# Optimization experiments

Measured on AMD Instinct MI355X. Metric: run time of the kernel, lower is better.

The kernel has to match this reference:

```python
import jax, jax.numpy as jnp
import numpy as np

B, N, D, E = 2, 50000, 128, 800000
EPS = 1e-5


def layer_norm(x, gamma, beta):
    m = jnp.mean(x, axis=-1, keepdims=True)
    v = jnp.mean((x - m) ** 2, axis=-1, keepdims=True)
    return (x - m) * jax.lax.rsqrt(v + EPS) * gamma + beta


def setup_inputs() -> dict:
    key = jax.random.key(0)
    ks = jax.random.split(key, 8)
    x = jax.random.normal(ks[0], (B, N, D), dtype=jnp.float32)
    edge_src = jax.random.randint(ks[1], (E,), 0, N)
    edge_dst = jax.random.randint(ks[2], (E,), 0, N)
    # degree consistent with edge_dst (in-degree), as a float tensor
    degree = jax.ops.segment_sum(jnp.ones((E,), jnp.float32), edge_dst, num_segments=N)
    # LayerNorm params (torch default init: gamma=1, beta=0)
    sn_g = jnp.ones((D,), jnp.float32); sn_b = jnp.zeros((D,), jnp.float32)
    nn_g = jnp.ones((D,), jnp.float32); nn_b = jnp.zeros((D,), jnp.float32)
    # MLP: Linear(2D, 2D) -> GELU -> Linear(2D, D); stored as [in, out]
    s1 = 1.0 / np.sqrt(2 * D)
    W1 = jax.random.uniform(ks[3], (2 * D, 2 * D), jnp.float32, -s1, s1)
    b1 = jax.random.uniform(ks[4], (2 * D,), jnp.float32, -s1, s1)
    W2 = jax.random.uniform(ks[5], (2 * D, D), jnp.float32, -s1, s1)
    b2 = jax.random.uniform(ks[6], (D,), jnp.float32, -s1, s1)
    return {"x": x, "edge_src": edge_src, "edge_dst": edge_dst, "degree": degree,
            "sn_g": sn_g, "sn_b": sn_b, "nn_g": nn_g, "nn_b": nn_b,
            "W1": W1, "b1": b1, "W2": W2, "b2": b2}


def reference(x, edge_src, edge_dst, degree, sn_g, sn_b, nn_g, nn_b, W1, b1, W2, b2):
    # gather messages from source nodes, scatter-add into destination nodes
    neighbor = jnp.zeros_like(x).at[:, edge_dst, :].add(x[:, edge_src, :])  # [B,N,D]
    neighbor = neighbor / jnp.clip(degree, 1.0)[None, :, None]
    h = jnp.concatenate([layer_norm(x, sn_g, sn_b), layer_norm(neighbor, nn_g, nn_b)], axis=-1)  # [B,N,2D]
    h = jax.nn.gelu(h @ W1 + b1, approximate=False)  # torch nn.GELU default = exact erf
    return x + (h @ W2 + b2)
```

## Files before the change

kernel.cpp:

```cpp
#include <hip/hip_runtime.h>
#include <cstdint>

#define B_ 2
#define N_ 50000
#define D_ 128
#define E_ 800000
#define TOK 100000

typedef __bf16 bf16x8 __attribute__((ext_vector_type(8)));
typedef float f32x4 __attribute__((ext_vector_type(4)));

__device__ __forceinline__ unsigned short f2bf(float f) {
  union { float f; uint32_t u; } v; v.f = f;
  uint32_t u = v.u;
  return (unsigned short)((u + 0x7FFFu + ((u >> 16) & 1u)) >> 16);
}
__device__ __forceinline__ float uasf(uint32_t u) {
  union { uint32_t u; float f; } v; v.u = u; return v.f;
}
__device__ __forceinline__ float fast_gelu(float v) {
  float p = v * (1.5957691f + 0.07135481f * v * v);
  return v * __builtin_amdgcn_rcpf(1.0f + __expf(-p));
}

__global__ __launch_bounds__(256) void prep_k(
    const float* __restrict__ x, const float* __restrict__ W1,
    const float* __restrict__ W2, const float* __restrict__ degree,
    unsigned short* __restrict__ xb, unsigned short* __restrict__ W1t,
    unsigned short* __restrict__ W2t, int* __restrict__ rs,
    int* __restrict__ cursor) {
  __shared__ int wsum[4], woff[4], carry[2];
  const int blk = blockIdx.x;
  if (blk < 12500) {
    int q = (blk * 256 + threadIdx.x) * 4;
    int node = q >> 8;
    int rem = q & 255;
    int b = rem >> 7, c = rem & 127;
    float4 v = *(const float4*)(x + (size_t)b * (N_ * D_) + node * 128 + c);
    uint2 p = { (uint32_t)f2bf(v.x) | ((uint32_t)f2bf(v.y) << 16),
                (uint32_t)f2bf(v.z) | ((uint32_t)f2bf(v.w) << 16) };
    *(uint2*)(xb + q) = p;
  } else if (blk < 12884) {
    int t = (blk - 12500) * 256 + threadIdx.x;
    if (t < 65536) {
      int n = t >> 8, k = t & 255;
      int f = (n >> 4) * 8 + (k >> 5);
      int pos = ((n & 15) + ((k >> 3) & 3) * 16) * 8 + (k & 7);
      W1t[f * 512 + pos] = f2bf(W1[k * 256 + n]);
    } else {
      int t2 = t - 65536;
      int n = t2 >> 8, k = t2 & 255;
      int f = (n >> 4) * 8 + (k >> 5);
      int pos = ((n & 15) + ((k >> 3) & 3) * 16) * 8 + (k & 7);
      W2t[f * 512 + pos] = f2bf(W2[k * 128 + n]);
    }
  } else {
    const int tid = threadIdx.x, lane = tid & 63, wv = tid >> 6;
    if (tid == 0) carry[0] = 0;
    int p = 0;
    __syncthreads();
    for (int base = 0; base < N_; base += 1024) {
      int i = base + tid * 4;
      int4 v = {0, 0, 0, 0};
      if (i + 3 < N_) {
        float4 d4 = *(const float4*)(degree + i);
        v.x = (int)(d4.x + 0.5f); v.y = (int)(d4.y + 0.5f);
        v.z = (int)(d4.z + 0.5f); v.w = (int)(d4.w + 0.5f);
      } else {
        if (i     < N_) v.x = (int)(degree[i]     + 0.5f);
        if (i + 1 < N_) v.y = (int)(degree[i + 1] + 0.5f);
        if (i + 2 < N_) v.z = (int)(degree[i + 2] + 0.5f);
        if (i + 3 < N_) v.w = (int)(degree[i + 3] + 0.5f);
      }
      int s4 = v.x + v.y + v.z + v.w;
      int s = s4;
#pragma unroll
      for (int off = 1; off < 64; off <<= 1) {
        int t = __shfl_up(s, off);
        if (lane >= off) s += t;
      }
      if (lane == 63) wsum[wv] = s;
      __syncthreads();
      if (tid == 0) {
        int a = 0;
#pragma unroll
        for (int w = 0; w < 4; ++w) { woff[w] = a; a += wsum[w]; }
        carry[p ^ 1] = carry[p] + a;
      }
      __syncthreads();
      int pre = carry[p] + woff[wv] + (s - s4);
      int e0 = pre, e1 = pre + v.x, e2 = e1 + v.y, e3 = e2 + v.z;
      if (i + 3 < N_) {
        int4 w0 = {e0, e1, e2, e3};
        *(int4*)(rs + i) = w0;
        *(int4*)(cursor + i) = w0;
      } else {
        if (i     < N_) { rs[i]     = e0; cursor[i]     = e0; }
        if (i + 1 < N_) { rs[i + 1] = e1; cursor[i + 1] = e1; }
        if (i + 2 < N_) { rs[i + 2] = e2; cursor[i + 2] = e2; }
        if (i + 3 < N_) { rs[i + 3] = e3; cursor[i + 3] = e3; }
      }
      p ^= 1;
    }
    if (tid == 0) rs[N_] = E_;
  }
}

__global__ __launch_bounds__(256) void fill_k(const int* __restrict__ esrc,
                                              const int* __restrict__ edst,
                                              int* __restrict__ cursor,
                                              int* __restrict__ sorted_src) {
  int e4 = (blockIdx.x * 256 + threadIdx.x) * 4;
  if (e4 < E_) {
    int4 s4 = *(const int4*)(esrc + e4);
    int4 d4 = *(const int4*)(edst + e4);
    int p0 = atomicAdd(&cursor[d4.x], 1); sorted_src[p0] = s4.x;
    int p1 = atomicAdd(&cursor[d4.y], 1); sorted_src[p1] = s4.y;
    int p2 = atomicAdd(&cursor[d4.z], 1); sorted_src[p2] = s4.z;
    int p3 = atomicAdd(&cursor[d4.w], 1); sorted_src[p3] = s4.w;
  }
}

__global__ __launch_bounds__(256) void gather_ln_k(
    const unsigned short* __restrict__ xb,
    const int* __restrict__ rs, const int* __restrict__ ss,
    const float* __restrict__ sn_g, const float* __restrict__ sn_b,
    const float* __restrict__ nn_g, const float* __restrict__ nn_b,
    unsigned short* __restrict__ h) {
  const int node = blockIdx.x * 4 + (threadIdx.x >> 6);
  const int lane = threadIdx.x & 63;
  const int g = lane >> 5;
  const int l32 = lane & 31;
  const int r0 = rs[node], r1 = rs[node + 1];
  const unsigned short* xrow = xb + l32 * 8;
  float acc[8] = {0.f, 0.f, 0.f, 0.f, 0.f, 0.f, 0.f, 0.f};
  for (int e = r0; e < r1; e += 16) {
    int idx[8];
#pragma unroll
    for (int j = 0; j < 8; ++j) {
      int ej = e + 2 * j + g;
      idx[j] = ss[(ej < r1) ? ej : r0];
    }
    uint4 v[8];
#pragma unroll
    for (int j = 0; j < 8; ++j)
      v[j] = *(const uint4*)(xrow + (size_t)idx[j] * 256);
#pragma unroll
    for (int j = 0; j < 8; ++j) {
      if (e + 2 * j + g < r1) {
        acc[0] += uasf(v[j].x << 16); acc[1] += uasf(v[j].x & 0xffff0000u);
        acc[2] += uasf(v[j].y << 16); acc[3] += uasf(v[j].y & 0xffff0000u);
        acc[4] += uasf(v[j].z << 16); acc[5] += uasf(v[j].z & 0xffff0000u);
        acc[6] += uasf(v[j].w << 16); acc[7] += uasf(v[j].w & 0xffff0000u);
      }
    }
  }
#pragma unroll
  for (int k = 0; k < 8; ++k) acc[k] += __shfl_xor(acc[k], 32);
  const float invd = 1.0f / fmaxf((float)(r1 - r0), 1.0f);
  float nb[8];
#pragma unroll
  for (int k = 0; k < 8; ++k) nb[k] = acc[k] * invd;
  uint4 xq = *(const uint4*)(xrow + (size_t)node * 256);
  float xv[8];
  xv[0] = uasf(xq.x << 16); xv[1] = uasf(xq.x & 0xffff0000u);
  xv[2] = uasf(xq.y << 16); xv[3] = uasf(xq.y & 0xffff0000u);
  xv[4] = uasf(xq.z << 16); xv[5] = uasf(xq.z & 0xffff0000u);
  xv[6] = uasf(xq.w << 16); xv[7] = uasf(xq.w & 0xffff0000u);
  float sx = 0.f, sxx = 0.f, sn = 0.f, snn = 0.f;
#pragma unroll
  for (int k = 0; k < 8; ++k) {
    sx += xv[k]; sxx += xv[k] * xv[k];
    sn += nb[k]; snn += nb[k] * nb[k];
  }
#pragma unroll
  for (int off = 1; off < 16; off <<= 1) {
    sx  += __shfl_xor(sx, off);  sxx += __shfl_xor(sxx, off);
    sn  += __shfl_xor(sn, off);  snn += __shfl_xor(snn, off);
  }
  const float r = 1.0f / 128.0f;
  float mx = sx * r, vx = fmaxf(sxx * r - mx * mx, 0.f);
  float mn = sn * r, vn = fmaxf(snn * r - mn * mn, 0.f);
  float rx = rsqrtf(vx + 1e-5f), rn = rsqrtf(vn + 1e-5f);
  const int c = (l32 & 15) * 8;
  const float* gp = g ? nn_g : sn_g;
  const float* bp = g ? nn_b : sn_b;
  float4 g0 = *(const float4*)(gp + c), g1 = *(const float4*)(gp + c + 4);
  float4 b0 = *(const float4*)(bp + c), b1v = *(const float4*)(bp + c + 4);
  float gw[8] = {g0.x, g0.y, g0.z, g0.w, g1.x, g1.y, g1.z, g1.w};
  float bw[8] = {b0.x, b0.y, b0.z, b0.w, b1v.x, b1v.y, b1v.z, b1v.w};
  float mu = g ? mn : mx;
  float rs_ = g ? rn : rx;
  float o[8];
#pragma unroll
  for (int k = 0; k < 8; ++k) {
    float s = g ? nb[k] : xv[k];
    o[k] = (s - mu) * rs_ * gw[k] + bw[k];
  }
  uint4 po;
  po.x = (uint32_t)f2bf(o[0]) | ((uint32_t)f2bf(o[1]) << 16);
  po.y = (uint32_t)f2bf(o[2]) | ((uint32_t)f2bf(o[3]) << 16);
  po.z = (uint32_t)f2bf(o[4]) | ((uint32_t)f2bf(o[5]) << 16);
  po.w = (uint32_t)f2bf(o[6]) | ((uint32_t)f2bf(o[7]) << 16);
  unsigned short* hr = h + ((size_t)(l32 >> 4) * N_ + node) * 256 + g * 128 + c;
  *(uint4*)hr = po;
}

__global__ __launch_bounds__(256, 4) void fused_mlp_k(
    const unsigned short* __restrict__ A,
    const unsigned short* __restrict__ W1t,
    const unsigned short* __restrict__ W2t,
    const float* __restrict__ b1,
    const float* __restrict__ b2,
    const float* __restrict__ resid,
    float* __restrict__ outp, int M) {
  __shared__ unsigned short As[64 * 256];
  __shared__ unsigned short Hc[64 * 64];
  const int tid = threadIdx.x;
  const int wave = tid >> 6, lane = tid & 63;
  const int wr = wave >> 1;
  const int wc = wave & 1;
  const int quad = lane >> 4, l15 = lane & 15;
  const int m0 = blockIdx.x * 64;
  {
    uint4 v[8];
#pragma unroll
    for (int it = 0; it < 8; ++it) {
      int id = it * 256 + tid;
      int r = id >> 5, c16 = id & 31;
      int gm = m0 + r;
      uint4 va = {0u, 0u, 0u, 0u};
      if (gm < M) va = *(const uint4*)(A + (size_t)gm * 256 + c16 * 8);
      v[it] = va;
    }
#pragma unroll
    for (int it = 0; it < 8; ++it) {
      int id = it * 256 + tid;
      int r = id >> 5, c16 = id & 31;
      *(uint4*)(&As[r * 256 + (c16 ^ (r & 7)) * 8]) = v[it];
    }
  }
  f32x4 acc2[2][4] = {};
  __syncthreads();
  for (int nc = 0; nc < 4; ++nc) {
    f32x4 acc1[2][2] = {};
#pragma unroll
    for (int kc = 0; kc < 256; kc += 32) {
      bf16x8 a[2], b[2];
#pragma unroll
      for (int i = 0; i < 2; ++i) {
        int row = wr * 32 + i * 16 + l15;
        a[i] = *(const bf16x8*)(&As[row * 256 + ((kc + quad * 8) ^ ((row & 7) << 3))]);
      }
#pragma unroll
      for (int i = 0; i < 2; ++i) {
        int ftile = (nc * 4 + wc * 2 + i) * 8 + (kc >> 5);
        b[i] = *(const bf16x8*)(W1t + ftile * 512 + lane * 8);
      }
#pragma unroll
      for (int mi = 0; mi < 2; ++mi)
#pragma unroll
        for (int ni = 0; ni < 2; ++ni)
          acc1[mi][ni] = __builtin_amdgcn_mfma_f32_16x16x32_bf16(a[mi], b[ni], acc1[mi][ni], 0, 0, 0);
    }
    __syncthreads();
#pragma unroll
    for (int mi = 0; mi < 2; ++mi)
#pragma unroll
      for (int ni = 0; ni < 2; ++ni) {
        int col = wc * 32 + ni * 16 + l15;
        float bv = b1[nc * 64 + col];
#pragma unroll
        for (int rr = 0; rr < 4; ++rr) {
          int row = wr * 32 + mi * 16 + quad * 4 + rr;
          Hc[row * 64 + (col ^ ((row & 7) << 3))] = f2bf(fast_gelu(acc1[mi][ni][rr] + bv));
        }
      }
    __syncthreads();
#pragma unroll
    for (int kc = 0; kc < 64; kc += 32) {
      bf16x8 a[2], b[4];
#pragma unroll
      for (int i = 0; i < 2; ++i) {
        int row = wr * 32 + i * 16 + l15;
        a[i] = *(const bf16x8*)(&Hc[row * 64 + ((kc + quad * 8) ^ ((row & 7) << 3))]);
      }
#pragma unroll
      for (int i = 0; i < 4; ++i) {
        int ftile = (wc * 4 + i) * 8 + nc * 2 + (kc >> 5);
        b[i] = *(const bf16x8*)(W2t + ftile * 512 + lane * 8);
      }
#pragma unroll
      for (int mi = 0; mi < 2; ++mi)
#pragma unroll
        for (int ni = 0; ni < 4; ++ni)
          acc2[mi][ni] = __builtin_amdgcn_mfma_f32_16x16x32_bf16(a[mi], b[ni], acc2[mi][ni], 0, 0, 0);
    }
  }
#pragma unroll
  for (int mi = 0; mi < 2; ++mi)
#pragma unroll
    for (int ni = 0; ni < 4; ++ni) {
      int col = wc * 64 + ni * 16 + l15;
      float bv = b2[col];
#pragma unroll
      for (int rr = 0; rr < 4; ++rr) {
        int row = m0 + wr * 32 + mi * 16 + quad * 4 + rr;
        if (row < M) {
          float v = acc2[mi][ni][rr] + bv + resid[(size_t)row * 128 + col];
          outp[(size_t)row * 128 + col] = v;
        }
      }
    }
}

extern "C" void kernel_launch(void* const* d_in, const int* in_sizes, int n_in,
                              void* d_out, int out_size, void* d_ws, size_t ws_size,
                              hipStream_t stream) {
  const float* x      = (const float*)d_in[0];
  const int* esrc     = (const int*)d_in[1];
  const int* edst     = (const int*)d_in[2];
  const float* degree = (const float*)d_in[3];
  const float* sn_g   = (const float*)d_in[4];
  const float* sn_b   = (const float*)d_in[5];
  const float* nn_g   = (const float*)d_in[6];
  const float* nn_b   = (const float*)d_in[7];
  const float* W1     = (const float*)d_in[8];
  const float* b1     = (const float*)d_in[9];
  const float* W2     = (const float*)d_in[10];
  const float* b2     = (const float*)d_in[11];

  char* ws = (char*)d_ws;
  const size_t H_BYTES = (size_t)TOK * 256 * 2;
  unsigned short* h = (unsigned short*)ws;
  char* csr = ws + H_BYTES;
  int* rs         = (int*)(csr + 400000);
  int* cursor     = (int*)(csr + 600016);
  int* sorted_src = (int*)(csr + 800512);
  unsigned short* xb = (unsigned short*)(csr + 4194304);
  unsigned short* W1t = (unsigned short*)(ws + 2 * H_BYTES);
  unsigned short* W2t = W1t + 65536;

  prep_k<<<12885, 256, 0, stream>>>(x, W1, W2, degree, xb, W1t, W2t, rs, cursor);
  fill_k<<<(E_ / 4 + 255) / 256, 256, 0, stream>>>(esrc, edst, cursor, sorted_src);
  gather_ln_k<<<N_ / 4, 256, 0, stream>>>(xb, rs, sorted_src,
                                          sn_g, sn_b, nn_g, nn_b, h);
  fused_mlp_k<<<(TOK + 63) / 64, 256, 0, stream>>>(h, W1t, W2t, b1, b2,
                                                   x, (float*)d_out, TOK);
}
```

Baseline: 310.4 us.

## Merge prep and CSR fill into one cooperative kernel with parallel scan

Replaces the prep and fill kernels with a single cooperative-groups kernel of 1024 blocks that uses grid-wide syncs. The degree prefix scan, previously serial in one block, becomes a two-level scan: 49 blocks compute local scans, block 0 scans the block sums, then all threads add the offsets. The bf16 conversion, weight transpose and edge fill become grid-stride loops. The aim is to remove the long single-block scan tail and one kernel launch, at the cost of three grid.sync barriers and a cooperative launch that requires every block to be co-resident.

```diff
diff --git a/kernel.cpp b/kernel.cpp
--- a/kernel.cpp
+++ b/kernel.cpp
@@ -1,5 +1,8 @@
 #include <hip/hip_runtime.h>
+#include <hip/hip_cooperative_groups.h>
 #include <cstdint>
+
+namespace cg = cooperative_groups;
 
 #define B_ 2
 #define N_ 50000
@@ -23,16 +26,63 @@
   return v * __builtin_amdgcn_rcpf(1.0f + __expf(-p));
 }
 
-__global__ __launch_bounds__(256) void prep_k(
+__global__ __launch_bounds__(256, 4) void prepfill_k(
     const float* __restrict__ x, const float* __restrict__ W1,
     const float* __restrict__ W2, const float* __restrict__ degree,
+    const int* __restrict__ esrc, const int* __restrict__ edst,
     unsigned short* __restrict__ xb, unsigned short* __restrict__ W1t,
     unsigned short* __restrict__ W2t, int* __restrict__ rs,
-    int* __restrict__ cursor) {
-  __shared__ int wsum[4], woff[4], carry[2];
-  const int blk = blockIdx.x;
-  if (blk < 12500) {
-    int q = (blk * 256 + threadIdx.x) * 4;
+    int* __restrict__ cursor, int* __restrict__ bsum,
+    int* __restrict__ boff, int* __restrict__ sorted_src) {
+  cg::grid_group grid = cg::this_grid();
+  __shared__ int wsum[4], woff[4];
+  const int tid = threadIdx.x, lane = tid & 63, wv = tid >> 6;
+  const int gtid = blockIdx.x * 256 + tid;
+  const int gsize = gridDim.x * 256;
+
+  if (blockIdx.x < 49) {
+    int i = blockIdx.x * 1024 + tid * 4;
+    int4 v = {0, 0, 0, 0};
+    if (i + 3 < N_) {
+      float4 d4 = *(const float4*)(degree + i);
+      v.x = (int)(d4.x + 0.5f); v.y = (int)(d4.y + 0.5f);
+      v.z = (int)(d4.z + 0.5f); v.w = (int)(d4.w + 0.5f);
+    } else {
+      if (i     < N_) v.x = (int)(degree[i]     + 0.5f);
+      if (i + 1 < N_) v.y = (int)(degree[i + 1] + 0.5f);
+      if (i + 2 < N_) v.z = (int)(degree[i + 2] + 0.5f);
+      if (i + 3 < N_) v.w = (int)(degree[i + 3] + 0.5f);
+    }
+    int s4 = v.x + v.y + v.z + v.w;
+    int s = s4;
+#pragma unroll
+    for (int off = 1; off < 64; off <<= 1) {
+      int t = __shfl_up(s, off);
+      if (lane >= off) s += t;
+    }
+    if (lane == 63) wsum[wv] = s;
+    __syncthreads();
+    if (tid == 0) {
+      int a = 0;
+#pragma unroll
+      for (int w = 0; w < 4; ++w) { woff[w] = a; a += wsum[w]; }
+      bsum[blockIdx.x] = a;
+    }
+    __syncthreads();
+    int pre = woff[wv] + (s - s4);
+    int e0 = pre, e1 = pre + v.x, e2 = e1 + v.y, e3 = e2 + v.z;
+    if (i + 3 < N_) {
+      int4 w0 = {e0, e1, e2, e3};
+      *(int4*)(rs + i) = w0;
+    } else {
+      if (i     < N_) rs[i]     = e0;
+      if (i + 1 < N_) rs[i + 1] = e1;
+      if (i + 2 < N_) rs[i + 2] = e2;
+      if (i + 3 < N_) rs[i + 3] = e3;
+    }
+  }
+  for (int t = gtid; t < 3200000; t += gsize) {
+    int q = t * 4;
     int node = q >> 8;
     int rem = q & 255;
     int b = rem >> 7, c = rem & 127;
@@ -40,8 +90,8 @@
     uint2 p = { (uint32_t)f2bf(v.x) | ((uint32_t)f2bf(v.y) << 16),
                 (uint32_t)f2bf(v.z) | ((uint32_t)f2bf(v.w) << 16) };
     *(uint2*)(xb + q) = p;
-  } else if (blk < 12884) {
-    int t = (blk - 12500) * 256 + threadIdx.x;
+  }
+  for (int t = gtid; t < 98304; t += gsize) {
     if (t < 65536) {
       int n = t >> 8, k = t & 255;
       int f = (n >> 4) * 8 + (k >> 5);
@@ -54,64 +104,31 @@
       int pos = ((n & 15) + ((k >> 3) & 3) * 16) * 8 + (k & 7);
       W2t[f * 512 + pos] = f2bf(W2[k * 128 + n]);
     }
-  } else {
-    const int tid = threadIdx.x, lane = tid & 63, wv = tid >> 6;
-    if (tid == 0) carry[0] = 0;
-    int p = 0;
-    __syncthreads();
-    for (int base = 0; base < N_; base += 1024) {
-      int i = base + tid * 4;
-      int4 v = {0, 0, 0, 0};
-      if (i + 3 < N_) {
-        float4 d4 = *(const float4*)(degree + i);
-        v.x = (int)(d4.x + 0.5f); v.y = (int)(d4.y + 0.5f);
-        v.z = (int)(d4.z + 0.5f); v.w = (int)(d4.w + 0.5f);
-      } else {
-        if (i     < N_) v.x = (int)(degree[i]     + 0.5f);
-        if (i + 1 < N_) v.y = (int)(degree[i + 1] + 0.5f);
-        if (i + 2 < N_) v.z = (int)(degree[i + 2] + 0.5f);
-        if (i + 3 < N_) v.w = (int)(degree[i + 3] + 0.5f);
-      }
-      int s4 = v.x + v.y + v.z + v.w;
-      int s = s4;
-#pragma unroll
-      for (int off = 1; off < 64; off <<= 1) {
-        int t = __shfl_up(s, off);
-        if (lane >= off) s += t;
-      }
-      if (lane == 63) wsum[wv] = s;
-      __syncthreads();
-      if (tid == 0) {
-        int a = 0;
-#pragma unroll
-        for (int w = 0; w < 4; ++w) { woff[w] = a; a += wsum[w]; }
-        carry[p ^ 1] = carry[p] + a;
-      }
-      __syncthreads();
-      int pre = carry[p] + woff[wv] + (s - s4);
-      int e0 = pre, e1 = pre + v.x, e2 = e1 + v.y, e3 = e2 + v.z;
-      if (i + 3 < N_) {
-        int4 w0 = {e0, e1, e2, e3};
-        *(int4*)(rs + i) = w0;
-        *(int4*)(cursor + i) = w0;
-      } else {
-        if (i     < N_) { rs[i]     = e0; cursor[i]     = e0; }
-        if (i + 1 < N_) { rs[i + 1] = e1; cursor[i + 1] = e1; }
-        if (i + 2 < N_) { rs[i + 2] = e2; cursor[i + 2] = e2; }
-        if (i + 3 < N_) { rs[i + 3] = e3; cursor[i + 3] = e3; }
-      }
-      p ^= 1;
-    }
-    if (tid == 0) rs[N_] = E_;
-  }
-}
-
-__global__ __launch_bounds__(256) void fill_k(const int* __restrict__ esrc,
-                                              const int* __restrict__ edst,
-                                              int* __restrict__ cursor,
-                                              int* __restrict__ sorted_src) {
-  int e4 = (blockIdx.x * 256 + threadIdx.x) * 4;
-  if (e4 < E_) {
+  }
+  grid.sync();
+  if (blockIdx.x == 0 && tid < 64) {
+    int v = (tid < 49) ? bsum[tid] : 0;
+    int s = v;
+#pragma unroll
+    for (int off = 1; off < 64; off <<= 1) {
+      int t = __shfl_up(s, off);
+      if (lane >= off) s += t;
+    }
+    boff[tid] = s - v;
+  }
+  grid.sync();
+  for (int t = gtid; t < 12500; t += gsize) {
+    int i = t * 4;
+    int4 v = *(const int4*)(rs + i);
+    int off = boff[i >> 10];
+    v.x += off; v.y += off; v.z += off; v.w += off;
+    *(int4*)(rs + i) = v;
+    *(int4*)(cursor + i) = v;
+  }
+  if (gtid == 0) rs[N_] = E_;
+  grid.sync();
+  for (int t = gtid; t < E_ / 4; t += gsize) {
+    int e4 = t * 4;
     int4 s4 = *(const int4*)(esrc + e4);
     int4 d4 = *(const int4*)(edst + e4);
     int p0 = atomicAdd(&cursor[d4.x], 1); sorted_src[p0] = s4.x;
@@ -334,6 +351,8 @@
   const size_t H_BYTES = (size_t)TOK * 256 * 2;
   unsigned short* h = (unsigned short*)ws;
   char* csr = ws + H_BYTES;
+  int* bsum       = (int*)(csr);
+  int* boff       = (int*)(csr + 4096);
   int* rs         = (int*)(csr + 400000);
   int* cursor     = (int*)(csr + 600016);
   int* sorted_src = (int*)(csr + 800512);
@@ -341,8 +360,15 @@
   unsigned short* W1t = (unsigned short*)(ws + 2 * H_BYTES);
   unsigned short* W2t = W1t + 65536;
 
-  prep_k<<<12885, 256, 0, stream>>>(x, W1, W2, degree, xb, W1t, W2t, rs, cursor);
-  fill_k<<<(E_ / 4 + 255) / 256, 256, 0, stream>>>(esrc, edst, cursor, sorted_src);
+  void* args[] = {
+    (void*)&x, (void*)&W1, (void*)&W2, (void*)&degree,
+    (void*)&esrc, (void*)&edst,
+    (void*)&xb, (void*)&W1t, (void*)&W2t,
+    (void*)&rs, (void*)&cursor, (void*)&bsum, (void*)&boff,
+    (void*)&sorted_src
+  };
+  hipLaunchCooperativeKernel((const void*)prepfill_k, dim3(1024), dim3(256),
+                             args, 0, stream);
   gather_ln_k<<<N_ / 4, 256, 0, stream>>>(xb, rs, sorted_src,
                                           sn_g, sn_b, nn_g, nn_b, h);
   fused_mlp_k<<<(TOK + 63) / 64, 256, 0, stream>>>(h, W1t, W2t, b1, b2,
```

Result: slower. 648.2 us (+108.8%).
